# Kernel tuning notes

Measured on AMD Instinct MI355X. Metric: run time of the kernel, lower is better.

Reference implementation:

```python
import jax, jax.numpy as jnp
import numpy as np
import math

D_MODEL, D_K, D_V, H = 512, 64, 64, 8

def setup_inputs() -> dict:
    key = jax.random.key(0)
    ks = jax.random.split(key, 8)
    B, L = 2, 4096
    q = jax.random.normal(ks[0], (B, L, D_MODEL), dtype=jnp.float32)
    k = jax.random.normal(ks[1], (B, L, D_MODEL), dtype=jnp.float32)
    v = jax.random.normal(ks[2], (B, L, D_MODEL), dtype=jnp.float32)
    attention_mask = jnp.ones((B, L), dtype=jnp.int32)
    s = 1.0 / math.sqrt(D_MODEL)
    Wq = jax.random.uniform(ks[3], (D_MODEL, H * D_K), dtype=jnp.float32, minval=-s, maxval=s)
    Wk = jax.random.uniform(ks[4], (D_MODEL, H * D_K), dtype=jnp.float32, minval=-s, maxval=s)
    Wv = jax.random.uniform(ks[5], (D_MODEL, H * D_V), dtype=jnp.float32, minval=-s, maxval=s)
    so = 1.0 / math.sqrt(H * D_V)
    Wo = jax.random.uniform(ks[6], (H * D_V, D_MODEL), dtype=jnp.float32, minval=-so, maxval=so)
    return {"q": q, "k": k, "v": v, "attention_mask": attention_mask,
            "Wq": Wq, "Wk": Wk, "Wv": Wv, "Wo": Wo}

def reference(q, k, v, attention_mask, Wq, Wk, Wv, Wo):
    B, L, _ = q.shape
    scale = 1.0 / math.sqrt(D_K)
    # project and split heads: [B, H, L, d]
    qh = (q @ Wq).reshape(B, L, H, D_K).transpose(0, 2, 1, 3)
    kh = (k @ Wk).reshape(B, L, H, D_K).transpose(0, 2, 1, 3)
    vh = (v @ Wv).reshape(B, L, H, D_V).transpose(0, 2, 1, 3)
    score = jnp.einsum('bhqd,bhkd->bhqk', qh, kh) * scale  # [B,H,L,L]
    mask = attention_mask[:, None, None, :]  # [B,1,1,L]
    score = jnp.where(mask == 0, -jnp.inf, score)
    attn = jax.nn.softmax(score, axis=-1)
    out = jnp.einsum('bhqk,bhkd->bhqd', attn, vh)
    out = out.transpose(0, 2, 1, 3).reshape(B, L, H * D_V)
    return out @ Wo
```

## Files before the change

### kernel.cpp

```cpp
#include <hip/hip_runtime.h>

typedef short bf16x8 __attribute__((ext_vector_type(8)));
typedef float f32x4 __attribute__((ext_vector_type(4)));
typedef unsigned short u16x8 __attribute__((ext_vector_type(8)));

static __device__ __forceinline__ unsigned short f2bf(float f) {
  unsigned int x = __builtin_bit_cast(unsigned int, f);
  x += 0x7FFFu + ((x >> 16) & 1u);
  return (unsigned short)(x >> 16);
}
static __device__ __forceinline__ unsigned int pk2bf(float a, float b) {
  unsigned int ia = __builtin_bit_cast(unsigned int, a) + 0x8000u;
  unsigned int ib = __builtin_bit_cast(unsigned int, b) + 0x8000u;
  return __builtin_amdgcn_perm(ib, ia, 0x07060302u);
}
static __device__ __forceinline__ void gl2lds16(const unsigned short* g, unsigned short* l) {
  __builtin_amdgcn_global_load_lds(
      (const __attribute__((address_space(1))) unsigned int*)g,
      (__attribute__((address_space(3))) unsigned int*)l, 16, 0, 0);
}

__global__ __launch_bounds__(256) void prep(const float* __restrict__ q, const float* __restrict__ k,
                                            const float* __restrict__ v,
                                            const float* __restrict__ Wq, const float* __restrict__ Wk,
                                            const float* __restrict__ Wv, const float* __restrict__ Wo,
                                            unsigned short* __restrict__ xbf,
                                            unsigned short* __restrict__ WT) {
  __shared__ __align__(16) float T[64 * 68];
  const int bid = blockIdx.x;
  const int tid = threadIdx.x;
  if (bid < 6144) {
    const int sec = bid / 2048;
    const float* src = (sec == 0) ? q : (sec == 1) ? k : v;
    int i = ((bid % 2048) * 256 + tid) * 8;
    int row = i >> 9, col = i & 511;
    float4 a = *(const float4*)(src + i);
    float4 b = *(const float4*)(src + i + 4);
    uint4 pk;
    pk.x = pk2bf(a.x, a.y); pk.y = pk2bf(a.z, a.w);
    pk.z = pk2bf(b.x, b.y); pk.w = pk2bf(b.z, b.w);
    *(uint4*)(xbf + (size_t)row * 1536 + sec * 512 + col) = pk;
  } else {
    const int w = bid - 6144;
    const int z = w >> 6;
    const float* W = (z == 0) ? Wq : (z == 1) ? Wk : (z == 2) ? Wv : Wo;
    unsigned short* out = WT + (size_t)z * 512 * 512;
    const int k0 = ((w >> 3) & 7) * 64, n0 = (w & 7) * 64;
#pragma unroll
    for (int i = 0; i < 4; ++i) {
      int chunk = i * 256 + tid;
      int row = chunk >> 4, fc = chunk & 15;
      *(float4*)(T + row * 68 + fc * 4) =
          *(const float4*)(W + (size_t)(k0 + row) * 512 + n0 + fc * 4);
    }
    __syncthreads();
#pragma unroll
    for (int i = 0; i < 2; ++i) {
      int chunk = i * 256 + tid;
      int nr = chunk >> 3, kc = chunk & 7;
      u16x8 vv;
#pragma unroll
      for (int j = 0; j < 8; ++j) vv[j] = f2bf(T[(kc * 8 + j) * 68 + nr]);
      *(u16x8*)(out + (size_t)(n0 + nr) * 512 + k0 + kc * 8) = vv;
    }
  }
}

__global__ __launch_bounds__(256) void gemm_qkv(const unsigned short* __restrict__ xbf,
                                                const unsigned short* __restrict__ Bt,
                                                unsigned short* __restrict__ C,
                                                float qscale) {
  __shared__ __align__(16) unsigned short Abuf[2][128 * 32];
  __shared__ __align__(16) unsigned short Bbuf[2][128 * 32];
  const int by = blockIdx.y;
  const unsigned short* A = xbf + (by >> 2) * 512;
  const float scale = (by < 4) ? qscale : 1.0f;
  const int tid = threadIdx.x;
  const int wid = tid >> 6, lane = tid & 63, quad = lane >> 4, li = lane & 15;
  const int bm = blockIdx.x * 128, bn = by * 128;
  const int wm = (wid & 1) * 64, wn = (wid >> 1) * 64;
  const unsigned short* ga[2]; int oa[2];
  const unsigned short* gb[2]; int obx[2];
#pragma unroll
  for (int i = 0; i < 2; ++i) {
    int lam = i * 256 + tid;
    int r = lam >> 2, c = (lam & 3) ^ (r & 3);
    ga[i] = A + (size_t)(bm + r) * 1536 + c * 8;
    oa[i] = lam * 8;
    gb[i] = Bt + (size_t)(bn + r) * 512 + c * 8;
    obx[i] = lam * 8;
  }
#pragma unroll
  for (int i = 0; i < 2; ++i) {
    gl2lds16(ga[i], &Abuf[0][oa[i]]); ga[i] += 32;
    gl2lds16(gb[i], &Bbuf[0][obx[i]]); gb[i] += 32;
  }
  f32x4 acc[4][4] = {};
  const int sw = li & 3;
  for (int s = 0; s < 16; ++s) {
    __syncthreads();
    if (s + 1 < 16) {
      int p = (s + 1) & 1;
#pragma unroll
      for (int i = 0; i < 2; ++i) {
        gl2lds16(ga[i], &Abuf[p][oa[i]]); ga[i] += 32;
        gl2lds16(gb[i], &Bbuf[p][obx[i]]); gb[i] += 32;
      }
    }
    const unsigned short* As = &Abuf[s & 1][0];
    const unsigned short* Bs = &Bbuf[s & 1][0];
    bf16x8 af[4], bfr[4];
#pragma unroll
    for (int t = 0; t < 4; ++t) {
      af[t]  = *(const bf16x8*)(As + (wm + t * 16 + li) * 32 + ((quad ^ sw) * 8));
      bfr[t] = *(const bf16x8*)(Bs + (wn + t * 16 + li) * 32 + ((quad ^ sw) * 8));
    }
#pragma unroll
    for (int mt = 0; mt < 4; ++mt)
#pragma unroll
      for (int nt = 0; nt < 4; ++nt)
        acc[mt][nt] = __builtin_amdgcn_mfma_f32_16x16x32_bf16(af[mt], bfr[nt], acc[mt][nt], 0, 0, 0);
  }
#pragma unroll
  for (int mt = 0; mt < 4; ++mt)
#pragma unroll
    for (int nt = 0; nt < 4; ++nt) {
      int r0 = bm + wm + mt * 16 + quad * 4;
      int c  = bn + wn + nt * 16 + li;
#pragma unroll
      for (int r = 0; r < 4; ++r)
        C[(size_t)(r0 + r) * 1536 + c] = f2bf(acc[mt][nt][r] * scale);
    }
}

__global__ __launch_bounds__(512) void kvfrag(const unsigned short* __restrict__ qkv,
                                              unsigned short* __restrict__ kfr,
                                              unsigned short* __restrict__ vfr) {
  __shared__ __align__(16) unsigned short Ksh[64 * 72];
  __shared__ __align__(16) unsigned short Vsh[64 * 72];
  const int kt = blockIdx.x, bh = blockIdx.y;
  const int b = bh >> 3, h = bh & 7;
  const int tid = threadIdx.x;
  {
    int row = tid >> 3, c8 = tid & 7;
    const unsigned short* src = qkv + (size_t)(b * 4096 + kt * 64 + row) * 1536 + h * 64 + c8 * 8;
    *(uint4*)(Ksh + row * 72 + c8 * 8) = *(const uint4*)(src + 512);
    *(uint4*)(Vsh + row * 72 + c8 * 8) = *(const uint4*)(src + 1024);
  }
  __syncthreads();
  const int fi = tid >> 6, l = tid & 63;
  const size_t obase = ((size_t)(bh * 64 + kt) * 8 + fi) * 512 + l * 8;
  {
    int kb = fi >> 1, dh = fi & 1;
    uint4 kf = *(const uint4*)(Ksh + (kb * 16 + (l & 15)) * 72 + (l >> 4) * 8 + dh * 32);
    *(uint4*)(kfr + obase) = kf;
  }
  {
    int dc = fi >> 1, kh = fi & 1;
    u16x8 vf;
#pragma unroll
    for (int j = 0; j < 8; ++j)
      vf[j] = Vsh[((l >> 4) * 8 + kh * 32 + j) * 72 + dc * 16 + (l & 15)];
    *(u16x8*)(vfr + obase) = vf;
  }
}

__global__ __launch_bounds__(512, 4) void attn(const unsigned short* __restrict__ qkv,
                                               const unsigned short* __restrict__ kfr,
                                               const unsigned short* __restrict__ vfr,
                                               const int* __restrict__ mask,
                                               float* __restrict__ O0, float* __restrict__ O1,
                                               float* __restrict__ Lb) {
  __shared__ __align__(16) unsigned short Psh[8][32 * 72];
  __shared__ __align__(16) unsigned short MskBits[256];
  const int qt = blockIdx.x, h = blockIdx.y, z = blockIdx.z;
  const int b = z >> 1, half = z & 1;
  const int t0 = half * 32;
  const int tid = threadIdx.x;
  const int wid = tid >> 6, lane = tid & 63, quad = lane >> 4, li = lane & 15;
  const size_t tok0 = (size_t)b * 4096;
  const int bh = b * 8 + h;

  if (tid < 256) {
    const int4* mp = (const int4*)(mask + b * 4096 + tid * 16);
    unsigned int bits = 0;
#pragma unroll
    for (int j = 0; j < 4; ++j) {
      int4 m4 = mp[j];
      bits |= (m4.x ? 1u : 0u) << (j * 4 + 0);
      bits |= (m4.y ? 1u : 0u) << (j * 4 + 1);
      bits |= (m4.z ? 1u : 0u) << (j * 4 + 2);
      bits |= (m4.w ? 1u : 0u) << (j * 4 + 3);
    }
    MskBits[tid] = (unsigned short)bits;
  }
  __syncthreads();

  const unsigned short* qpa = qkv + (tok0 + qt * 256 + wid * 32 + li) * 1536 + h * 64;
  const unsigned short* qpb = qpa + 16 * 1536;
  bf16x8 bq0a = *(const bf16x8*)(qpa + quad * 8);
  bf16x8 bq1a = *(const bf16x8*)(qpa + 32 + quad * 8);
  bf16x8 bq0b = *(const bf16x8*)(qpb + quad * 8);
  bf16x8 bq1b = *(const bf16x8*)(qpb + 32 + quad * 8);

  const unsigned short* kbp = kfr + ((size_t)(bh * 64 + t0) * 8) * 512 + lane * 8;
  const unsigned short* vbp = vfr + ((size_t)(bh * 64 + t0) * 8) * 512 + lane * 8;

  f32x4 accOa[4] = {}, accOb[4] = {};
  f32x4 accLa = {}, accLb = {};
  bf16x8 bones;
#pragma unroll
  for (int j = 0; j < 8; ++j) bones[j] = (short)0x3F80;
  unsigned short* Pw = &Psh[wid][0];

  for (int tt = 0; tt < 32; ++tt) {
    const int t = t0 + tt;
    bf16x8 kf[8];
#pragma unroll
    for (int fi = 0; fi < 8; ++fi) kf[fi] = *(const bf16x8*)(kbp + fi * 512);
    f32x4 sa[4], sb[4];
#pragma unroll
    for (int kb = 0; kb < 4; ++kb) {
      f32x4 za = {}, zb = {};
      za = __builtin_amdgcn_mfma_f32_16x16x32_bf16(kf[kb * 2], bq0a, za, 0, 0, 0);
      za = __builtin_amdgcn_mfma_f32_16x16x32_bf16(kf[kb * 2 + 1], bq1a, za, 0, 0, 0);
      zb = __builtin_amdgcn_mfma_f32_16x16x32_bf16(kf[kb * 2], bq0b, zb, 0, 0, 0);
      zb = __builtin_amdgcn_mfma_f32_16x16x32_bf16(kf[kb * 2 + 1], bq1b, zb, 0, 0, 0);
      sa[kb] = za; sb[kb] = zb;
    }
    unsigned long long mbits = *(const unsigned long long*)(MskBits + t * 4);
    if (mbits != ~0ull) {
#pragma unroll
      for (int kb = 0; kb < 4; ++kb)
#pragma unroll
        for (int r = 0; r < 4; ++r) {
          int key = kb * 16 + quad * 4 + r;
          if (!((mbits >> key) & 1ull)) { sa[kb][r] = -1e30f; sb[kb][r] = -1e30f; }
        }
    }
#pragma unroll
    for (int kb = 0; kb < 4; ++kb) {
#pragma unroll
      for (int r = 0; r < 4; ++r) {
        sa[kb][r] = __builtin_amdgcn_exp2f(sa[kb][r]);
        sb[kb][r] = __builtin_amdgcn_exp2f(sb[kb][r]);
      }
      uint2 pka, pkb;
      pka.x = pk2bf(sa[kb][0], sa[kb][1]); pka.y = pk2bf(sa[kb][2], sa[kb][3]);
      pkb.x = pk2bf(sb[kb][0], sb[kb][1]); pkb.y = pk2bf(sb[kb][2], sb[kb][3]);
      *(uint2*)(Pw + li * 72 + kb * 16 + quad * 4) = pka;
      *(uint2*)(Pw + (li + 16) * 72 + kb * 16 + quad * 4) = pkb;
    }
    bf16x8 p0a = *(const bf16x8*)(Pw + li * 72 + quad * 8);
    bf16x8 p1a = *(const bf16x8*)(Pw + li * 72 + 32 + quad * 8);
    bf16x8 p0b = *(const bf16x8*)(Pw + (li + 16) * 72 + quad * 8);
    bf16x8 p1b = *(const bf16x8*)(Pw + (li + 16) * 72 + 32 + quad * 8);
#pragma unroll
    for (int dc = 0; dc < 4; ++dc) {
      bf16x8 bv0 = *(const bf16x8*)(vbp + (dc * 2) * 512);
      bf16x8 bv1 = *(const bf16x8*)(vbp + (dc * 2 + 1) * 512);
      accOa[dc] = __builtin_amdgcn_mfma_f32_16x16x32_bf16(p0a, bv0, accOa[dc], 0, 0, 0);
      accOa[dc] = __builtin_amdgcn_mfma_f32_16x16x32_bf16(p1a, bv1, accOa[dc], 0, 0, 0);
      accOb[dc] = __builtin_amdgcn_mfma_f32_16x16x32_bf16(p0b, bv0, accOb[dc], 0, 0, 0);
      accOb[dc] = __builtin_amdgcn_mfma_f32_16x16x32_bf16(p1b, bv1, accOb[dc], 0, 0, 0);
    }
    accLa = __builtin_amdgcn_mfma_f32_16x16x32_bf16(p0a, bones, accLa, 0, 0, 0);
    accLa = __builtin_amdgcn_mfma_f32_16x16x32_bf16(p1a, bones, accLa, 0, 0, 0);
    accLb = __builtin_amdgcn_mfma_f32_16x16x32_bf16(p0b, bones, accLb, 0, 0, 0);
    accLb = __builtin_amdgcn_mfma_f32_16x16x32_bf16(p1b, bones, accLb, 0, 0, 0);
    kbp += 8 * 512;
    vbp += 8 * 512;
  }
  float* Oh = half ? O1 : O0;
  const size_t rqa = tok0 + qt * 256 + wid * 32 + quad * 4;
  const size_t rqb = rqa + 16;
#pragma unroll
  for (int dc = 0; dc < 4; ++dc) {
    size_t col = h * 64 + dc * 16 + li;
#pragma unroll
    for (int r = 0; r < 4; ++r) {
      Oh[(rqa + r) * 512 + col] = accOa[dc][r];
      Oh[(rqb + r) * 512 + col] = accOb[dc][r];
    }
  }
  if (li == 0) {
#pragma unroll
    for (int r = 0; r < 4; ++r) {
      Lb[((size_t)half * 8192 + rqa + r) * 8 + h] = accLa[r];
      Lb[((size_t)half * 8192 + rqb + r) * 8 + h] = accLb[r];
    }
  }
}

__global__ __launch_bounds__(256) void cmb(const float* __restrict__ O0, const float* __restrict__ O1,
                                           const float* __restrict__ Lb,
                                           unsigned short* __restrict__ ob) {
  int idx = (blockIdx.x * 256 + threadIdx.x) * 4;
  int tok = idx >> 9, h = (idx >> 6) & 7;
  float inv = 1.f / (Lb[(size_t)tok * 8 + h] + Lb[(size_t)(8192 + tok) * 8 + h]);
  float4 a = *(const float4*)(O0 + idx);
  float4 b = *(const float4*)(O1 + idx);
  uint2 pk;
  pk.x = pk2bf((a.x + b.x) * inv, (a.y + b.y) * inv);
  pk.y = pk2bf((a.z + b.z) * inv, (a.w + b.w) * inv);
  *(uint2*)(ob + idx) = pk;
}

__global__ __launch_bounds__(256) void gemm_o(const unsigned short* __restrict__ A,
                                              const unsigned short* __restrict__ Bt,
                                              float* __restrict__ Cf) {
  __shared__ __align__(16) unsigned short Abuf[2][128 * 64];
  __shared__ __align__(16) unsigned short Bbuf[2][64 * 64];
  const int K = 512, LDC = 512;
  const int tid = threadIdx.x;
  const int wid = tid >> 6, lane = tid & 63, quad = lane >> 4, li = lane & 15;
  const int bm = blockIdx.x * 128, bn = blockIdx.y * 64;
  const int wm = wid * 32;
  const unsigned short* ga[4]; int oa[4];
  const unsigned short* gb[2]; int ob[2];
#pragma unroll
  for (int i = 0; i < 4; ++i) {
    int lam = i * 256 + wid * 64 + lane;
    int r = lam >> 3, c = (lam & 7) ^ (r & 7);
    ga[i] = A + (size_t)(bm + r) * K + c * 8;
    oa[i] = lam * 8;
  }
#pragma unroll
  for (int i = 0; i < 2; ++i) {
    int lam = i * 256 + wid * 64 + lane;
    int r = lam >> 3, c = (lam & 7) ^ (r & 7);
    gb[i] = Bt + (size_t)(bn + r) * K + c * 8;
    ob[i] = lam * 8;
  }
#pragma unroll
  for (int i = 0; i < 4; ++i) { gl2lds16(ga[i], &Abuf[0][oa[i]]); ga[i] += 64; }
#pragma unroll
  for (int i = 0; i < 2; ++i) { gl2lds16(gb[i], &Bbuf[0][ob[i]]); gb[i] += 64; }

  f32x4 acc[2][4] = {};
  const int sw = li & 7;
  for (int s = 0; s < 8; ++s) {
    __syncthreads();
    if (s + 1 < 8) {
      int p = (s + 1) & 1;
#pragma unroll
      for (int i = 0; i < 4; ++i) { gl2lds16(ga[i], &Abuf[p][oa[i]]); ga[i] += 64; }
#pragma unroll
      for (int i = 0; i < 2; ++i) { gl2lds16(gb[i], &Bbuf[p][ob[i]]); gb[i] += 64; }
    }
    const unsigned short* As = &Abuf[s & 1][0];
    const unsigned short* Bs = &Bbuf[s & 1][0];
#pragma unroll
    for (int kk = 0; kk < 2; ++kk) {
      bf16x8 af[2], bfr[4];
#pragma unroll
      for (int t = 0; t < 2; ++t)
        af[t] = *(const bf16x8*)(As + (wm + t * 16 + li) * 64 + (((kk * 4 + quad) ^ sw) * 8));
#pragma unroll
      for (int t = 0; t < 4; ++t)
        bfr[t] = *(const bf16x8*)(Bs + (t * 16 + li) * 64 + (((kk * 4 + quad) ^ sw) * 8));
#pragma unroll
      for (int mt = 0; mt < 2; ++mt)
#pragma unroll
        for (int nt = 0; nt < 4; ++nt)
          acc[mt][nt] = __builtin_amdgcn_mfma_f32_16x16x32_bf16(af[mt], bfr[nt], acc[mt][nt], 0, 0, 0);
    }
  }
#pragma unroll
  for (int mt = 0; mt < 2; ++mt)
#pragma unroll
    for (int nt = 0; nt < 4; ++nt) {
      int r0 = bm + wm + mt * 16 + quad * 4;
      int c  = bn + nt * 16 + li;
#pragma unroll
      for (int r = 0; r < 4; ++r)
        Cf[(size_t)(r0 + r) * LDC + c] = acc[mt][nt][r];
    }
}

extern "C" void kernel_launch(void* const* d_in, const int* in_sizes, int n_in,
                              void* d_out, int out_size, void* d_ws, size_t ws_size,
                              hipStream_t stream) {
  const float* q  = (const float*)d_in[0];
  const float* k  = (const float*)d_in[1];
  const float* v  = (const float*)d_in[2];
  const int* mask = (const int*)d_in[3];
  const float* Wq = (const float*)d_in[4];
  const float* Wk = (const float*)d_in[5];
  const float* Wv = (const float*)d_in[6];
  const float* Wo = (const float*)d_in[7];
  float* out = (float*)d_out;

  char* ws = (char*)d_ws;
  const size_t MB = 1024 * 1024;
  unsigned short* kfr  = (unsigned short*)(ws);
  unsigned short* vfr  = (unsigned short*)(ws + 16 * MB);
  unsigned short* qkvh = (unsigned short*)(ws + 32 * MB);
  unsigned short* xbf  = (unsigned short*)(ws + 56 * MB);
  float* O0f = (float*)(ws + 56 * MB);
  float* O1f = (float*)(ws + 72 * MB);
  float* Lb  = (float*)(ws + 88 * MB);
  unsigned short* wAll = (unsigned short*)(ws + 89 * MB);
  unsigned short* woT  = wAll + (size_t)3 * 512 * 512;
  unsigned short* obb  = (unsigned short*)(ws);

  prep<<<6400, 256, 0, stream>>>(q, k, v, Wq, Wk, Wv, Wo, xbf, wAll);
  const float qscale = 0.125f * 1.44269504f;
  dim3 gq(64, 12);
  gemm_qkv<<<gq, 256, 0, stream>>>(xbf, wAll, qkvh, qscale);
  dim3 fg(64, 16);
  kvfrag<<<fg, 512, 0, stream>>>(qkvh, kfr, vfr);
  dim3 ag(16, 8, 4);
  attn<<<ag, 512, 0, stream>>>(qkvh, kfr, vfr, mask, O0f, O1f, Lb);
  cmb<<<4096, 256, 0, stream>>>(O0f, O1f, Lb, obb);
  dim3 go(64, 8);
  gemm_o<<<go, 256, 0, stream>>>(obb, woT, out);
}
```

Before: 237.4 us.

## Feed P to PV MFMA from registers via 16x16x16 bf16, drop LDS round-trip

The softmax probability tile P is no longer written to shared memory and re-read in the A-operand layout. Instead the accumulator layout of the QK MFMA is used directly as the A operand of 16x16x16 bf16 MFMAs, and the V fragment packing in the prep kernel is rearranged to match the new k-ordering. This removes per-iteration LDS stores and loads and the per-wave P buffer. In exchange it issues twice as many smaller MFMA instructions, which may have lower throughput per FLOP than the 16x16x32 form.

New measurement: 241.7 us. No clear change (+1.8%).

```diff
diff --git a/kernel.cpp b/kernel.cpp
--- a/kernel.cpp
+++ b/kernel.cpp
@@ -1,6 +1,7 @@
 #include <hip/hip_runtime.h>
 
 typedef short bf16x8 __attribute__((ext_vector_type(8)));
+typedef short bf16x4 __attribute__((ext_vector_type(4)));
 typedef float f32x4 __attribute__((ext_vector_type(4)));
 typedef unsigned short u16x8 __attribute__((ext_vector_type(8)));
 
@@ -18,6 +19,16 @@
   __builtin_amdgcn_global_load_lds(
       (const __attribute__((address_space(1))) unsigned int*)g,
       (__attribute__((address_space(3))) unsigned int*)l, 16, 0, 0);
+}
+static __device__ __forceinline__ f32x4 mfma16(bf16x4 a, bf16x4 b, f32x4 c) {
+#if __has_builtin(__builtin_amdgcn_mfma_f32_16x16x16_bf16)
+  return __builtin_amdgcn_mfma_f32_16x16x16_bf16(a, b, c, 0, 0, 0);
+#elif __has_builtin(__builtin_amdgcn_mfma_f32_16x16x16bf16_1k)
+  return __builtin_amdgcn_mfma_f32_16x16x16bf16_1k(a, b, c, 0, 0, 0);
+#else
+  asm("v_mfma_f32_16x16x16_bf16 %0, %1, %2, %0" : "+v"(c) : "v"(a), "v"(b));
+  return c;
+#endif
 }
 
 __global__ __launch_bounds__(256) void prep(const float* __restrict__ q, const float* __restrict__ k,
@@ -156,11 +167,13 @@
     *(uint4*)(kfr + obase) = kf;
   }
   {
-    int dc = fi >> 1, kh = fi & 1;
+    int dc = fi >> 1, c = fi & 1;
     u16x8 vf;
 #pragma unroll
-    for (int j = 0; j < 8; ++j)
-      vf[j] = Vsh[((l >> 4) * 8 + kh * 32 + j) * 72 + dc * 16 + (l & 15)];
+    for (int j = 0; j < 4; ++j) {
+      vf[j]     = Vsh[(32 * c + (l >> 4) * 4 + j) * 72 + dc * 16 + (l & 15)];
+      vf[4 + j] = Vsh[(32 * c + 16 + (l >> 4) * 4 + j) * 72 + dc * 16 + (l & 15)];
+    }
     *(u16x8*)(vfr + obase) = vf;
   }
 }
@@ -171,7 +184,6 @@
                                                const int* __restrict__ mask,
                                                float* __restrict__ O0, float* __restrict__ O1,
                                                float* __restrict__ Lb) {
-  __shared__ __align__(16) unsigned short Psh[8][32 * 72];
   __shared__ __align__(16) unsigned short MskBits[256];
   const int qt = blockIdx.x, h = blockIdx.y, z = blockIdx.z;
   const int b = z >> 1, half = z & 1;
@@ -208,10 +220,9 @@
 
   f32x4 accOa[4] = {}, accOb[4] = {};
   f32x4 accLa = {}, accLb = {};
-  bf16x8 bones;
-#pragma unroll
-  for (int j = 0; j < 8; ++j) bones[j] = (short)0x3F80;
-  unsigned short* Pw = &Psh[wid][0];
+  bf16x4 bones4;
+#pragma unroll
+  for (int j = 0; j < 4; ++j) bones4[j] = (short)0x3F80;
 
   for (int tt = 0; tt < 32; ++tt) {
     const int t = t0 + tt;
@@ -238,6 +249,7 @@
           if (!((mbits >> key) & 1ull)) { sa[kb][r] = -1e30f; sb[kb][r] = -1e30f; }
         }
     }
+    bf16x4 pa[4], pb[4];
 #pragma unroll
     for (int kb = 0; kb < 4; ++kb) {
 #pragma unroll
@@ -245,29 +257,34 @@
         sa[kb][r] = __builtin_amdgcn_exp2f(sa[kb][r]);
         sb[kb][r] = __builtin_amdgcn_exp2f(sb[kb][r]);
       }
-      uint2 pka, pkb;
-      pka.x = pk2bf(sa[kb][0], sa[kb][1]); pka.y = pk2bf(sa[kb][2], sa[kb][3]);
-      pkb.x = pk2bf(sb[kb][0], sb[kb][1]); pkb.y = pk2bf(sb[kb][2], sb[kb][3]);
-      *(uint2*)(Pw + li * 72 + kb * 16 + quad * 4) = pka;
-      *(uint2*)(Pw + (li + 16) * 72 + kb * 16 + quad * 4) = pkb;
-    }
-    bf16x8 p0a = *(const bf16x8*)(Pw + li * 72 + quad * 8);
-    bf16x8 p1a = *(const bf16x8*)(Pw + li * 72 + 32 + quad * 8);
-    bf16x8 p0b = *(const bf16x8*)(Pw + (li + 16) * 72 + quad * 8);
-    bf16x8 p1b = *(const bf16x8*)(Pw + (li + 16) * 72 + 32 + quad * 8);
+      uint2 ua, ub;
+      ua.x = pk2bf(sa[kb][0], sa[kb][1]); ua.y = pk2bf(sa[kb][2], sa[kb][3]);
+      ub.x = pk2bf(sb[kb][0], sb[kb][1]); ub.y = pk2bf(sb[kb][2], sb[kb][3]);
+      pa[kb] = __builtin_bit_cast(bf16x4, ua);
+      pb[kb] = __builtin_bit_cast(bf16x4, ub);
+    }
+#pragma unroll
+    for (int kb = 0; kb < 4; ++kb) {
+      accLa = mfma16(pa[kb], bones4, accLa);
+      accLb = mfma16(pb[kb], bones4, accLb);
+    }
 #pragma unroll
     for (int dc = 0; dc < 4; ++dc) {
-      bf16x8 bv0 = *(const bf16x8*)(vbp + (dc * 2) * 512);
-      bf16x8 bv1 = *(const bf16x8*)(vbp + (dc * 2 + 1) * 512);
-      accOa[dc] = __builtin_amdgcn_mfma_f32_16x16x32_bf16(p0a, bv0, accOa[dc], 0, 0, 0);
-      accOa[dc] = __builtin_amdgcn_mfma_f32_16x16x32_bf16(p1a, bv1, accOa[dc], 0, 0, 0);
-      accOb[dc] = __builtin_amdgcn_mfma_f32_16x16x32_bf16(p0b, bv0, accOb[dc], 0, 0, 0);
-      accOb[dc] = __builtin_amdgcn_mfma_f32_16x16x32_bf16(p1b, bv1, accOb[dc], 0, 0, 0);
-    }
-    accLa = __builtin_amdgcn_mfma_f32_16x16x32_bf16(p0a, bones, accLa, 0, 0, 0);
-    accLa = __builtin_amdgcn_mfma_f32_16x16x32_bf16(p1a, bones, accLa, 0, 0, 0);
-    accLb = __builtin_amdgcn_mfma_f32_16x16x32_bf16(p0b, bones, accLb, 0, 0, 0);
-    accLb = __builtin_amdgcn_mfma_f32_16x16x32_bf16(p1b, bones, accLb, 0, 0, 0);
+      bf16x8 vv0 = *(const bf16x8*)(vbp + (dc * 2) * 512);
+      bf16x8 vv1 = *(const bf16x8*)(vbp + (dc * 2 + 1) * 512);
+      bf16x4 v0 = __builtin_shufflevector(vv0, vv0, 0, 1, 2, 3);
+      bf16x4 v1 = __builtin_shufflevector(vv0, vv0, 4, 5, 6, 7);
+      bf16x4 v2 = __builtin_shufflevector(vv1, vv1, 0, 1, 2, 3);
+      bf16x4 v3 = __builtin_shufflevector(vv1, vv1, 4, 5, 6, 7);
+      accOa[dc] = mfma16(pa[0], v0, accOa[dc]);
+      accOa[dc] = mfma16(pa[1], v1, accOa[dc]);
+      accOa[dc] = mfma16(pa[2], v2, accOa[dc]);
+      accOa[dc] = mfma16(pa[3], v3, accOa[dc]);
+      accOb[dc] = mfma16(pb[0], v0, accOb[dc]);
+      accOb[dc] = mfma16(pb[1], v1, accOb[dc]);
+      accOb[dc] = mfma16(pb[2], v2, accOb[dc]);
+      accOb[dc] = mfma16(pb[3], v3, accOb[dc]);
+    }
     kbp += 8 * 512;
     vbp += 8 * 512;
   }
```
